# Optimization experiments

Measured on AMD Instinct MI355X. Metric: run time of the kernel, lower is better.

The kernel has to match this reference:

```python
import jax, jax.numpy as jnp
import numpy as np

S = 16        # neighbor samples per layer
NL = 2        # number of GNN layers


def setup_inputs() -> dict:
    key = jax.random.key(0)
    ks = jax.random.split(key, 12)
    N_NODES, D, E, NMP, DEG, N_EDGE, B, NC = 50000, 128, 32, 3, 32, 200000, 1024, 8
    sc = 0.05
    return {
        "ids": jax.random.randint(ks[0], (B,), 0, N_NODES, dtype=jnp.int32),
        "feats": jax.random.normal(ks[1], (N_NODES, D), jnp.float32),
        "edge_emb": jax.random.normal(ks[2], (NMP, N_EDGE, E), jnp.float32),
        "adj_nodes": jax.random.randint(ks[3], (NMP, N_NODES, DEG), 0, N_NODES, dtype=jnp.int32),
        "adj_edges": jax.random.randint(ks[4], (NMP, N_NODES, DEG), 0, N_EDGE, dtype=jnp.int32),
        "W_self": jax.random.normal(ks[5], (NMP, NL, D, D), jnp.float32) * sc,
        "W_neigh": jax.random.normal(ks[6], (NMP, NL, D + E, D), jnp.float32) * sc,
        "W_edge": jax.random.normal(ks[7], (NMP, NL, 2 * D + E, E), jnp.float32) * sc,
        "attn": jax.random.normal(ks[8], (D,), jnp.float32) * sc,
        "fc_w": jax.random.normal(ks[9], (D, NC), jnp.float32) * sc,
        "fc_b": jnp.zeros((NC,), jnp.float32),
    }


def reference(ids, feats, edge_emb, adj_nodes, adj_edges, W_self, W_neigh, W_edge, attn, fc_w, fc_b):
    NMP = adj_nodes.shape[0]
    outs = []
    for mp in range(NMP):
        # --- sample neighbor tree (deterministic: first S columns) ---
        cur = ids
        all_feats = [feats[cur]]
        all_edges = []
        for _ in range(NL):
            nb = adj_nodes[mp][cur][:, :S].reshape(-1)     # [N*S]
            eid = adj_edges[mp][cur][:, :S].reshape(-1)    # [N*S]
            all_edges.append(edge_emb[mp][eid])            # [N*S, E]
            cur = nb
            all_feats.append(feats[cur])
        # --- per-layer aggregation + edge update ---
        for l in range(NL):
            new_feats = []
            for k in range(len(all_feats) - 1):
                xs, xn, ee = all_feats[k], all_feats[k + 1], all_edges[k]
                N = xs.shape[0]
                # mean over sampled neighbors of [neigh_feat || edge_emb]
                nin = jnp.concatenate(
                    [xn.reshape(N, S, -1), ee.reshape(N, S, -1)], axis=-1
                ).mean(axis=1)                             # [N, D+E]
                new_feats.append(jax.nn.relu(xs @ W_self[mp, l] + nin @ W_neigh[mp, l]))
            all_feats = new_feats  # dropout is identity in eval mode
            new_edges = []
            for k in range(len(all_edges) - 1):
                xs, xn, ee = all_feats[k], all_feats[k + 1], all_edges[k]
                rep = jnp.repeat(xs, S, axis=0)            # [N*S, D]
                new_edges.append(jax.nn.relu(
                    jnp.concatenate([rep, xn, ee], axis=-1) @ W_edge[mp, l]))
            all_edges = new_edges
        outs.append(all_feats[0])                          # [B, D]
    stacked = jnp.stack(outs)                              # [NMP, B, D]
    # metapath attention fuse
    scores = jnp.tanh(jnp.einsum('mbd,d->mb', stacked, attn))
    beta = jax.nn.softmax(scores, axis=0)
    emb = jnp.einsum('mb,mbd->bd', beta, stacked)          # [B, D]
    # F.normalize(dim=1)
    emb = emb / jnp.maximum(jnp.linalg.norm(emb, axis=1, keepdims=True), 1e-12)
    return emb @ fc_w + fc_b
```

## Files before the change

### kernel.cpp

```cpp
#include <hip/hip_runtime.h>

#define NNODES  50000
#define D       128
#define E       32
#define NMP     3
#define DEG     32
#define NEDGE   200000
#define B       1024
#define NC      8
#define S       16

#define RPM      17408
#define NKT      9
#define WSTRIDE  36864
#define WESTRIDE 9216

typedef float f4 __attribute__((ext_vector_type(4)));
typedef short bh8 __attribute__((ext_vector_type(8)));

static __device__ __forceinline__ unsigned short f2bf(float f) {
    unsigned int u = __float_as_uint(f);
    u = u + 0x7FFFu + ((u >> 16) & 1u);
    return (unsigned short)(u >> 16);
}
static __device__ __forceinline__ float bf2f(unsigned short h) {
    return __uint_as_float(((unsigned int)h) << 16);
}

__global__ __launch_bounds__(256) void convert_k(
    const float* __restrict__ feats, const float* __restrict__ Ws,
    const float* __restrict__ Wn, const float* __restrict__ We,
    unsigned short* __restrict__ fb, unsigned short* __restrict__ WT0,
    unsigned short* __restrict__ WTe)
{
    int i = blockIdx.x * 256 + threadIdx.x;
    if (i < 1600000) {
        float4 v = ((const float4*)feats)[i];
        unsigned int p0 = (unsigned int)f2bf(v.x) | ((unsigned int)f2bf(v.y) << 16);
        unsigned int p1 = (unsigned int)f2bf(v.z) | ((unsigned int)f2bf(v.w) << 16);
        ((uint2*)fb)[i] = make_uint2(p0, p1);
    } else if (i < 1600000 + 6 * WSTRIDE) {
        int i2 = i - 1600000;
        int ml = i2 / WSTRIDE, e = i2 % WSTRIDE;
        int j = e & 7, t1 = e >> 3;
        int n = t1 & 127, t2 = t1 >> 7;
        int q = t2 & 3, kt = t2 >> 2;
        int k = kt * 32 + q * 8 + j;
        float v = (k < 128) ? Ws[((size_t)ml * 128 + k) * 128 + n]
                            : Wn[((size_t)ml * 160 + (k - 128)) * 128 + n];
        WT0[(size_t)ml * WSTRIDE + e] = f2bf(v);
    } else if (i < 1600000 + 6 * WSTRIDE + 3 * WESTRIDE) {
        int i3 = i - 1600000 - 6 * WSTRIDE;
        int mp = i3 / WESTRIDE, e = i3 % WESTRIDE;
        int j = e & 7, t1 = e >> 3;
        int n = t1 & 31, t2 = t1 >> 5;
        int q = t2 & 3, kt = t2 >> 2;
        int k = kt * 32 + q * 8 + j;
        float v = We[(((size_t)mp * 2) * 288 + k) * 32 + n];
        WTe[(size_t)mp * WESTRIDE + e] = f2bf(v);
    }
}

__global__ __launch_bounds__(256) void sample_k(
    const int* __restrict__ ids, const int* __restrict__ adjn,
    const int* __restrict__ adje, int* __restrict__ gx, int* __restrict__ eid1)
{
    int mp = blockIdx.y;
    int i = blockIdx.x * 256 + threadIdx.x;
    const int* an = adjn + (size_t)mp * NNODES * DEG;
    const int* ae = adje + (size_t)mp * NNODES * DEG;
    if (i < 16384) {
        int node = ids[i >> 4];
        gx[mp * RPM + i]     = an[(size_t)node * DEG + (i & 15)];
        eid1[mp * 16384 + i] = ae[(size_t)node * DEG + (i & 15)];
    } else if (i < RPM) {
        gx[mp * RPM + i] = ids[i - 16384];
    }
}

__global__ __launch_bounds__(256) void aggnin_k(
    const unsigned short* __restrict__ fb, const float* __restrict__ edge_emb,
    const int* __restrict__ adjn, const int* __restrict__ adje,
    const int* __restrict__ gx, const int* __restrict__ eid1,
    unsigned short* __restrict__ nin)
{
    const int mp = blockIdx.y;
    const int r = blockIdx.x * 4 + (threadIdx.x >> 6);
    const int t = threadIdx.x & 63;
    const float* ee = edge_emb + (size_t)mp * NEDGE * E;

    const int* ip;
    const int* eix;
    if (r < 16384) {
        int node = __builtin_amdgcn_readfirstlane(gx[mp * RPM + r]);
        ip  = adjn + ((size_t)mp * NNODES + node) * DEG;
        eix = adje + ((size_t)mp * NNODES + node) * DEG;
    } else {
        ip  = gx + mp * RPM + (r - 16384) * S;
        eix = eid1 + mp * 16384 + (r - 16384) * S;
    }

    const int hi = t >> 5, t31 = t & 31;

    unsigned int fv[S];
#pragma unroll
    for (int j = 0; j < S; ++j) {
        int nb = __builtin_amdgcn_readfirstlane(ip[j]);
        fv[j] = ((const unsigned int*)fb)[(size_t)nb * 64 + t];
    }
    float ev[S / 2];
#pragma unroll
    for (int e = 0; e < S / 2; ++e) {
        int e_ev = __builtin_amdgcn_readfirstlane(eix[2 * e]);
        int e_od = __builtin_amdgcn_readfirstlane(eix[2 * e + 1]);
        int edd = hi ? e_od : e_ev;
        ev[e] = ee[(size_t)edd * E + t31];
    }

    float s0 = 0.f, s1 = 0.f, se = 0.f;
#pragma unroll
    for (int j = 0; j < S; ++j) {
        s0 += bf2f((unsigned short)(fv[j] & 0xFFFF));
        s1 += bf2f((unsigned short)(fv[j] >> 16));
    }
#pragma unroll
    for (int e = 0; e < S / 2; ++e) se += ev[e];
    se += __shfl_xor(se, 32);

    const float inv = 1.0f / (float)S;
    unsigned short* row = nin + ((size_t)mp * RPM + r) * 160;
    ((unsigned int*)row)[t] =
        (unsigned int)f2bf(s0 * inv) | ((unsigned int)f2bf(s1 * inv) << 16);
    if (t < E) row[128 + t] = f2bf(se * inv);
}

__global__ __launch_bounds__(256) void gemm_feat_k(
    const unsigned short* __restrict__ fb, const int* __restrict__ gx,
    const unsigned short* __restrict__ fout_in,
    const unsigned short* __restrict__ nin,
    const unsigned short* __restrict__ WT0,
    unsigned short* __restrict__ outb, float* __restrict__ outf, int mode)
{
    const int mp = blockIdx.y;
    const int w = threadIdx.x >> 6;
    const int l = threadIdx.x & 63;
    const int q = l >> 4, lm = l & 15;
    const int m0 = blockIdx.x * 128 + w * 32;
    const int ninStride = mode ? B : RPM;
    const unsigned short* wb = WT0 + ((size_t)mp * 2 + mode) * WSTRIDE;

    const unsigned short* ap[2];
    const unsigned short* np[2];
#pragma unroll
    for (int mt = 0; mt < 2; ++mt) {
        int row = m0 + mt * 16 + lm;
        if (mode == 0) {
            int node = gx[mp * RPM + row];
            ap[mt] = fb + (size_t)node * 128;
        } else {
            ap[mt] = fout_in + ((size_t)mp * RPM + 16384 + row) * 128;
        }
        np[mt] = nin + ((size_t)mp * ninStride + row) * 160;
    }

    f4 acc[2][8];
#pragma unroll
    for (int mt = 0; mt < 2; ++mt)
#pragma unroll
        for (int nt = 0; nt < 8; ++nt) acc[mt][nt] = (f4){0.f, 0.f, 0.f, 0.f};

#pragma unroll
    for (int kt = 0; kt < NKT; ++kt) {
        const int k0 = kt * 32 + q * 8;
        bh8 a[2];
#pragma unroll
        for (int mt = 0; mt < 2; ++mt) {
            const unsigned short* p = (k0 < 128) ? (ap[mt] + k0) : (np[mt] + (k0 - 128));
            a[mt] = *(const bh8*)p;
        }
        const unsigned short* wrow = wb + ((size_t)(kt * 4 + q) * 128 + lm) * 8;
#pragma unroll
        for (int nt = 0; nt < 8; ++nt) {
            bh8 bf = *(const bh8*)(wrow + nt * 16 * 8);
#pragma unroll
            for (int mt = 0; mt < 2; ++mt)
                acc[mt][nt] = __builtin_amdgcn_mfma_f32_16x16x32_bf16(a[mt], bf, acc[mt][nt], 0, 0, 0);
        }
    }

    if (mode == 0) {
#pragma unroll
        for (int mt = 0; mt < 2; ++mt)
#pragma unroll
            for (int nt = 0; nt < 8; ++nt)
#pragma unroll
                for (int rr = 0; rr < 4; ++rr) {
                    int row = m0 + mt * 16 + q * 4 + rr;
                    int col = nt * 16 + lm;
                    outb[((size_t)mp * RPM + row) * 128 + col] = f2bf(fmaxf(acc[mt][nt][rr], 0.f));
                }
    } else {
#pragma unroll
        for (int mt = 0; mt < 2; ++mt)
#pragma unroll
            for (int nt = 0; nt < 8; ++nt)
#pragma unroll
                for (int rr = 0; rr < 4; ++rr) {
                    int row = m0 + mt * 16 + q * 4 + rr;
                    int col = nt * 16 + lm;
                    outf[((size_t)mp * B + row) * 128 + col] = fmaxf(acc[mt][nt][rr], 0.f);
                }
    }
}

__global__ __launch_bounds__(256) void gemm_edge_k(
    const unsigned short* __restrict__ fout, const float* __restrict__ edge_emb,
    const int* __restrict__ eid1, const unsigned short* __restrict__ WTe,
    unsigned short* __restrict__ e0p)
{
    const int mp = blockIdx.y;
    const int w = threadIdx.x >> 6, l = threadIdx.x & 63;
    const int q = l >> 4, lm = l & 15;
    const int m0 = blockIdx.x * 128 + w * 32;
    const unsigned short* we = WTe + (size_t)mp * WESTRIDE;
    const unsigned short* f1base = fout + (size_t)mp * RPM * 128;
    const unsigned short* f0base = fout + ((size_t)mp * RPM + 16384) * 128;
    const float* ee = edge_emb + (size_t)mp * NEDGE * E;

    const unsigned short* a1p[2];
    const unsigned short* a0p[2];
    int eidL[2];
#pragma unroll
    for (int mt = 0; mt < 2; ++mt) {
        int row = m0 + mt * 16 + lm;
        a1p[mt] = f1base + (size_t)row * 128;
        a0p[mt] = f0base + (size_t)(row >> 4) * 128;
        eidL[mt] = eid1[mp * 16384 + row];
    }

    f4 acc[2][2];
#pragma unroll
    for (int mt = 0; mt < 2; ++mt) { acc[mt][0] = (f4){0,0,0,0}; acc[mt][1] = (f4){0,0,0,0}; }

#pragma unroll
    for (int kt = 0; kt < NKT; ++kt) {
        const int k0 = kt * 32 + q * 8;
        bh8 a[2];
#pragma unroll
        for (int mt = 0; mt < 2; ++mt) {
            if (kt < 4) {
                a[mt] = *(const bh8*)(a0p[mt] + k0);
            } else if (kt < 8) {
                a[mt] = *(const bh8*)(a1p[mt] + (k0 - 128));
            } else {
                const float* ep = ee + (size_t)eidL[mt] * E + q * 8;
                float4 v0 = *(const float4*)ep;
                float4 v1 = *(const float4*)(ep + 4);
                bh8 tv;
                tv[0] = (short)f2bf(v0.x); tv[1] = (short)f2bf(v0.y);
                tv[2] = (short)f2bf(v0.z); tv[3] = (short)f2bf(v0.w);
                tv[4] = (short)f2bf(v1.x); tv[5] = (short)f2bf(v1.y);
                tv[6] = (short)f2bf(v1.z); tv[7] = (short)f2bf(v1.w);
                a[mt] = tv;
            }
        }
        const unsigned short* wrow = we + ((size_t)(kt * 4 + q) * 32 + lm) * 8;
        bh8 b0 = *(const bh8*)(wrow);
        bh8 b1 = *(const bh8*)(wrow + 16 * 8);
#pragma unroll
        for (int mt = 0; mt < 2; ++mt) {
            acc[mt][0] = __builtin_amdgcn_mfma_f32_16x16x32_bf16(a[mt], b0, acc[mt][0], 0, 0, 0);
            acc[mt][1] = __builtin_amdgcn_mfma_f32_16x16x32_bf16(a[mt], b1, acc[mt][1], 0, 0, 0);
        }
    }
#pragma unroll
    for (int mt = 0; mt < 2; ++mt)
#pragma unroll
        for (int nt = 0; nt < 2; ++nt)
#pragma unroll
            for (int rr = 0; rr < 4; ++rr) {
                int row = m0 + mt * 16 + q * 4 + rr;
                int col = nt * 16 + lm;
                e0p[((size_t)mp * 16384 + row) * 32 + col] = f2bf(fmaxf(acc[mt][nt][rr], 0.f));
            }
}

__global__ __launch_bounds__(256) void aggseq_k(
    const unsigned short* __restrict__ fout, const unsigned short* __restrict__ e0p,
    unsigned short* __restrict__ agg1)
{
    int mp = blockIdx.y;
    int bRow = blockIdx.x * 4 + (threadIdx.x >> 6);
    int t = threadIdx.x & 63;
    const unsigned short* f1 = fout + ((size_t)mp * RPM + (size_t)bRow * 16) * 128;
    const unsigned short* e0 = e0p + ((size_t)mp * 16384 + (size_t)bRow * 16) * 32;
    float s0 = 0.f, s1 = 0.f, se = 0.f;
#pragma unroll
    for (int j = 0; j < S; ++j) {
        unsigned int u = ((const unsigned int*)(f1 + j * 128))[t];
        s0 += bf2f((unsigned short)(u & 0xFFFF));
        s1 += bf2f((unsigned short)(u >> 16));
        if (t < E) se += bf2f(e0[j * 32 + t]);
    }
    const float inv = 1.0f / (float)S;
    unsigned short* row = agg1 + ((size_t)mp * B + bRow) * 160;
    ((unsigned int*)row)[t] =
        (unsigned int)f2bf(s0 * inv) | ((unsigned int)f2bf(s1 * inv) << 16);
    if (t < E) row[128 + t] = f2bf(se * inv);
}

__global__ __launch_bounds__(64) void finalize_k(
    const float* __restrict__ outs,
    const float* __restrict__ attn, const float* __restrict__ fcw,
    const float* __restrict__ fcb, float* __restrict__ out)
{
    const int b = blockIdx.x;
    const int t = threadIdx.x;
    float v0[NMP], v1[NMP], sc[NMP];
    float at0 = attn[t], at1 = attn[64 + t];
#pragma unroll
    for (int mp = 0; mp < NMP; ++mp) {
        v0[mp] = outs[((size_t)mp * B + b) * D + t];
        v1[mp] = outs[((size_t)mp * B + b) * D + 64 + t];
        float p = v0[mp] * at0 + v1[mp] * at1;
#pragma unroll
        for (int off = 32; off; off >>= 1) p += __shfl_xor(p, off);
        sc[mp] = tanhf(p);
    }
    float mx = fmaxf(sc[0], fmaxf(sc[1], sc[2]));
    float e0 = expf(sc[0] - mx), e1 = expf(sc[1] - mx), e2 = expf(sc[2] - mx);
    float isum = 1.f / (e0 + e1 + e2);
    float b0 = e0 * isum, b1 = e1 * isum, b2 = e2 * isum;
    float emb0 = b0 * v0[0] + b1 * v0[1] + b2 * v0[2];
    float emb1 = b0 * v1[0] + b1 * v1[1] + b2 * v1[2];
    float nn = emb0 * emb0 + emb1 * emb1;
#pragma unroll
    for (int off = 32; off; off >>= 1) nn += __shfl_xor(nn, off);
    float innorm = 1.f / fmaxf(sqrtf(nn), 1e-12f);
    emb0 *= innorm; emb1 *= innorm;
    float pc[NC];
#pragma unroll
    for (int c = 0; c < NC; ++c) {
        float p = emb0 * fcw[t * NC + c] + emb1 * fcw[(64 + t) * NC + c];
#pragma unroll
        for (int off = 32; off; off >>= 1) p += __shfl_xor(p, off);
        pc[c] = p;
    }
    if (t == 0) {
#pragma unroll
        for (int c = 0; c < NC; ++c)
            out[(size_t)b * NC + c] = pc[c] + fcb[c];
    }
}

extern "C" void kernel_launch(void* const* d_in, const int* in_sizes, int n_in,
                              void* d_out, int out_size, void* d_ws, size_t ws_size,
                              hipStream_t stream) {
    const int* ids        = (const int*)d_in[0];
    const float* feats    = (const float*)d_in[1];
    const float* edge_emb = (const float*)d_in[2];
    const int* adjn       = (const int*)d_in[3];
    const int* adje       = (const int*)d_in[4];
    const float* Ws       = (const float*)d_in[5];
    const float* Wn       = (const float*)d_in[6];
    const float* We       = (const float*)d_in[7];
    const float* attn     = (const float*)d_in[8];
    const float* fcw      = (const float*)d_in[9];
    const float* fcb      = (const float*)d_in[10];
    float* out = (float*)d_out;

    char* p = (char*)d_ws;
    unsigned short* WT0 = (unsigned short*)p; p += (size_t)6 * WSTRIDE * 2;
    unsigned short* WTe = (unsigned short*)p; p += (size_t)3 * WESTRIDE * 2;
    unsigned short* fb  = (unsigned short*)p; p += (size_t)NNODES * 128 * 2;
    int* gx   = (int*)p;                      p += (size_t)3 * RPM * 4;
    int* eid1 = (int*)p;                      p += (size_t)3 * 16384 * 4;
    unsigned short* nin  = (unsigned short*)p; p += (size_t)3 * RPM * 160 * 2;
    unsigned short* fout = (unsigned short*)p; p += (size_t)3 * RPM * 128 * 2;
    unsigned short* e0p  = (unsigned short*)p; p += (size_t)3 * 16384 * 32 * 2;
    unsigned short* agg1 = (unsigned short*)p; p += (size_t)3 * B * 160 * 2;
    float* outs = (float*)p;                   p += (size_t)3 * B * 128 * 4;

    convert_k<<<7222, 256, 0, stream>>>(feats, Ws, Wn, We, fb, WT0, WTe);
    sample_k<<<dim3(68, 3), 256, 0, stream>>>(ids, adjn, adje, gx, eid1);
    aggnin_k<<<dim3(RPM / 4, 3), 256, 0, stream>>>(fb, edge_emb, adjn, adje, gx, eid1, nin);
    gemm_feat_k<<<dim3(136, 3), 256, 0, stream>>>(fb, gx, fout, nin, WT0, fout, nullptr, 0);
    gemm_edge_k<<<dim3(128, 3), 256, 0, stream>>>(fout, edge_emb, eid1, WTe, e0p);
    aggseq_k<<<dim3(256, 3), 256, 0, stream>>>(fout, e0p, agg1);
    gemm_feat_k<<<dim3(8, 3), 256, 0, stream>>>(fb, nullptr, fout, agg1, WT0, nullptr, outs, 1);
    finalize_k<<<B, 64, 0, stream>>>(outs, attn, fcw, fcb, out);
}
```

Baseline: 248.2 us.

## Fuse pipeline stages to cut kernel launches and intermediate buffers

Merges weight/feature conversion with neighbor sampling into one launch. Folds the edge-GEMM output straight into the mean aggregation, so the e0p intermediate buffer is never written. Combines the final layer's feature GEMM with the attention, normalize and FC finalize step through shared memory, dropping the outs buffer. This goes from eight launches to five and removes intermediate global traffic, but the final fused kernel runs only 32 blocks, which limits parallelism on that stage.

```diff
diff --git a/kernel.cpp b/kernel.cpp
--- a/kernel.cpp
+++ b/kernel.cpp
@@ -15,6 +15,9 @@
 #define WSTRIDE  36864
 #define WESTRIDE 9216
 
+#define CONV_TASKS (1600000 + 6 * WSTRIDE + 3 * WESTRIDE)
+#define TOT_TASKS  (CONV_TASKS + 3 * RPM)
+
 typedef float f4 __attribute__((ext_vector_type(4)));
 typedef short bh8 __attribute__((ext_vector_type(8)));
 
@@ -27,11 +30,13 @@
     return __uint_as_float(((unsigned int)h) << 16);
 }
 
-__global__ __launch_bounds__(256) void convert_k(
+__global__ __launch_bounds__(256) void convsamp_k(
     const float* __restrict__ feats, const float* __restrict__ Ws,
     const float* __restrict__ Wn, const float* __restrict__ We,
+    const int* __restrict__ ids, const int* __restrict__ adjn,
+    const int* __restrict__ adje,
     unsigned short* __restrict__ fb, unsigned short* __restrict__ WT0,
-    unsigned short* __restrict__ WTe)
+    unsigned short* __restrict__ WTe, int* __restrict__ gx, int* __restrict__ eid1)
 {
     int i = blockIdx.x * 256 + threadIdx.x;
     if (i < 1600000) {
@@ -49,7 +54,7 @@
         float v = (k < 128) ? Ws[((size_t)ml * 128 + k) * 128 + n]
                             : Wn[((size_t)ml * 160 + (k - 128)) * 128 + n];
         WT0[(size_t)ml * WSTRIDE + e] = f2bf(v);
-    } else if (i < 1600000 + 6 * WSTRIDE + 3 * WESTRIDE) {
+    } else if (i < CONV_TASKS) {
         int i3 = i - 1600000 - 6 * WSTRIDE;
         int mp = i3 / WESTRIDE, e = i3 % WESTRIDE;
         int j = e & 7, t1 = e >> 3;
@@ -58,23 +63,16 @@
         int k = kt * 32 + q * 8 + j;
         float v = We[(((size_t)mp * 2) * 288 + k) * 32 + n];
         WTe[(size_t)mp * WESTRIDE + e] = f2bf(v);
-    }
-}
-
-__global__ __launch_bounds__(256) void sample_k(
-    const int* __restrict__ ids, const int* __restrict__ adjn,
-    const int* __restrict__ adje, int* __restrict__ gx, int* __restrict__ eid1)
-{
-    int mp = blockIdx.y;
-    int i = blockIdx.x * 256 + threadIdx.x;
-    const int* an = adjn + (size_t)mp * NNODES * DEG;
-    const int* ae = adje + (size_t)mp * NNODES * DEG;
-    if (i < 16384) {
-        int node = ids[i >> 4];
-        gx[mp * RPM + i]     = an[(size_t)node * DEG + (i & 15)];
-        eid1[mp * 16384 + i] = ae[(size_t)node * DEG + (i & 15)];
-    } else if (i < RPM) {
-        gx[mp * RPM + i] = ids[i - 16384];
+    } else if (i < TOT_TASKS) {
+        int i4 = i - CONV_TASKS;
+        int mp = i4 / RPM, r = i4 % RPM;
+        if (r < 16384) {
+            int node = ids[r >> 4];
+            gx[mp * RPM + r]   = adjn[((size_t)mp * NNODES + node) * DEG + (r & 15)];
+            eid1[mp * 16384 + r] = adje[((size_t)mp * NNODES + node) * DEG + (r & 15)];
+        } else {
+            gx[mp * RPM + r] = ids[r - 16384];
+        }
     }
 }
 
@@ -136,31 +134,25 @@
 
 __global__ __launch_bounds__(256) void gemm_feat_k(
     const unsigned short* __restrict__ fb, const int* __restrict__ gx,
-    const unsigned short* __restrict__ fout_in,
     const unsigned short* __restrict__ nin,
     const unsigned short* __restrict__ WT0,
-    unsigned short* __restrict__ outb, float* __restrict__ outf, int mode)
+    unsigned short* __restrict__ outb)
 {
     const int mp = blockIdx.y;
     const int w = threadIdx.x >> 6;
     const int l = threadIdx.x & 63;
     const int q = l >> 4, lm = l & 15;
     const int m0 = blockIdx.x * 128 + w * 32;
-    const int ninStride = mode ? B : RPM;
-    const unsigned short* wb = WT0 + ((size_t)mp * 2 + mode) * WSTRIDE;
+    const unsigned short* wb = WT0 + (size_t)mp * 2 * WSTRIDE;
 
     const unsigned short* ap[2];
     const unsigned short* np[2];
 #pragma unroll
     for (int mt = 0; mt < 2; ++mt) {
         int row = m0 + mt * 16 + lm;
-        if (mode == 0) {
-            int node = gx[mp * RPM + row];
-            ap[mt] = fb + (size_t)node * 128;
-        } else {
-            ap[mt] = fout_in + ((size_t)mp * RPM + 16384 + row) * 128;
-        }
-        np[mt] = nin + ((size_t)mp * ninStride + row) * 160;
+        int node = gx[mp * RPM + row];
+        ap[mt] = fb + (size_t)node * 128;
+        np[mt] = nin + ((size_t)mp * RPM + row) * 160;
     }
 
     f4 acc[2][8];
@@ -188,35 +180,22 @@
         }
     }
 
-    if (mode == 0) {
-#pragma unroll
-        for (int mt = 0; mt < 2; ++mt)
-#pragma unroll
-            for (int nt = 0; nt < 8; ++nt)
-#pragma unroll
-                for (int rr = 0; rr < 4; ++rr) {
-                    int row = m0 + mt * 16 + q * 4 + rr;
-                    int col = nt * 16 + lm;
-                    outb[((size_t)mp * RPM + row) * 128 + col] = f2bf(fmaxf(acc[mt][nt][rr], 0.f));
-                }
-    } else {
-#pragma unroll
-        for (int mt = 0; mt < 2; ++mt)
-#pragma unroll
-            for (int nt = 0; nt < 8; ++nt)
-#pragma unroll
-                for (int rr = 0; rr < 4; ++rr) {
-                    int row = m0 + mt * 16 + q * 4 + rr;
-                    int col = nt * 16 + lm;
-                    outf[((size_t)mp * B + row) * 128 + col] = fmaxf(acc[mt][nt][rr], 0.f);
-                }
-    }
-}
-
-__global__ __launch_bounds__(256) void gemm_edge_k(
+#pragma unroll
+    for (int mt = 0; mt < 2; ++mt)
+#pragma unroll
+        for (int nt = 0; nt < 8; ++nt)
+#pragma unroll
+            for (int rr = 0; rr < 4; ++rr) {
+                int row = m0 + mt * 16 + q * 4 + rr;
+                int col = nt * 16 + lm;
+                outb[((size_t)mp * RPM + row) * 128 + col] = f2bf(fmaxf(acc[mt][nt][rr], 0.f));
+            }
+}
+
+__global__ __launch_bounds__(256) void edgeagg_k(
     const unsigned short* __restrict__ fout, const float* __restrict__ edge_emb,
     const int* __restrict__ eid1, const unsigned short* __restrict__ WTe,
-    unsigned short* __restrict__ e0p)
+    unsigned short* __restrict__ agg1)
 {
     const int mp = blockIdx.y;
     const int w = threadIdx.x >> 6, l = threadIdx.x & 63;
@@ -226,6 +205,7 @@
     const unsigned short* f1base = fout + (size_t)mp * RPM * 128;
     const unsigned short* f0base = fout + ((size_t)mp * RPM + 16384) * 128;
     const float* ee = edge_emb + (size_t)mp * NEDGE * E;
+    const float inv = 1.0f / (float)S;
 
     const unsigned short* a1p[2];
     const unsigned short* a0p[2];
@@ -273,83 +253,116 @@
             acc[mt][1] = __builtin_amdgcn_mfma_f32_16x16x32_bf16(a[mt], b1, acc[mt][1], 0, 0, 0);
         }
     }
-#pragma unroll
-    for (int mt = 0; mt < 2; ++mt)
-#pragma unroll
-        for (int nt = 0; nt < 2; ++nt)
-#pragma unroll
-            for (int rr = 0; rr < 4; ++rr) {
-                int row = m0 + mt * 16 + q * 4 + rr;
-                int col = nt * 16 + lm;
-                e0p[((size_t)mp * 16384 + row) * 32 + col] = f2bf(fmaxf(acc[mt][nt][rr], 0.f));
-            }
-}
-
-__global__ __launch_bounds__(256) void aggseq_k(
-    const unsigned short* __restrict__ fout, const unsigned short* __restrict__ e0p,
-    unsigned short* __restrict__ agg1)
-{
-    int mp = blockIdx.y;
-    int bRow = blockIdx.x * 4 + (threadIdx.x >> 6);
-    int t = threadIdx.x & 63;
-    const unsigned short* f1 = fout + ((size_t)mp * RPM + (size_t)bRow * 16) * 128;
-    const unsigned short* e0 = e0p + ((size_t)mp * 16384 + (size_t)bRow * 16) * 32;
-    float s0 = 0.f, s1 = 0.f, se = 0.f;
-#pragma unroll
-    for (int j = 0; j < S; ++j) {
-        unsigned int u = ((const unsigned int*)(f1 + j * 128))[t];
-        s0 += bf2f((unsigned short)(u & 0xFFFF));
-        s1 += bf2f((unsigned short)(u >> 16));
-        if (t < E) se += bf2f(e0[j * 32 + t]);
-    }
-    const float inv = 1.0f / (float)S;
-    unsigned short* row = agg1 + ((size_t)mp * B + bRow) * 160;
-    ((unsigned int*)row)[t] =
-        (unsigned int)f2bf(s0 * inv) | ((unsigned int)f2bf(s1 * inv) << 16);
-    if (t < E) row[128 + t] = f2bf(se * inv);
-}
-
-__global__ __launch_bounds__(64) void finalize_k(
-    const float* __restrict__ outs,
+
+#pragma unroll
+    for (int mt = 0; mt < 2; ++mt) {
+        int seg = (m0 >> 4) + mt;
+#pragma unroll
+        for (int nt = 0; nt < 2; ++nt) {
+            float ps = 0.f;
+#pragma unroll
+            for (int rr = 0; rr < 4; ++rr) ps += fmaxf(acc[mt][nt][rr], 0.f);
+            ps += __shfl_xor(ps, 16);
+            ps += __shfl_xor(ps, 32);
+            if (l < 16)
+                agg1[((size_t)mp * B + seg) * 160 + 128 + nt * 16 + lm] = f2bf(ps * inv);
+        }
+    }
+
+#pragma unroll
+    for (int mt = 0; mt < 2; ++mt) {
+        int seg = (m0 >> 4) + mt;
+        const unsigned short* fr = f1base + (size_t)seg * 16 * 128;
+        float s0 = 0.f, s1 = 0.f;
+#pragma unroll
+        for (int j = 0; j < S; ++j) {
+            unsigned int u = ((const unsigned int*)(fr + j * 128))[l];
+            s0 += bf2f((unsigned short)(u & 0xFFFF));
+            s1 += bf2f((unsigned short)(u >> 16));
+        }
+        ((unsigned int*)(agg1 + ((size_t)mp * B + seg) * 160))[l] =
+            (unsigned int)f2bf(s0 * inv) | ((unsigned int)f2bf(s1 * inv) << 16);
+    }
+}
+
+__global__ __launch_bounds__(256) void feat1fin_k(
+    const unsigned short* __restrict__ fout, const unsigned short* __restrict__ agg1,
+    const unsigned short* __restrict__ WT0,
     const float* __restrict__ attn, const float* __restrict__ fcw,
     const float* __restrict__ fcb, float* __restrict__ out)
 {
-    const int b = blockIdx.x;
-    const int t = threadIdx.x;
-    float v0[NMP], v1[NMP], sc[NMP];
-    float at0 = attn[t], at1 = attn[64 + t];
+    __shared__ float sbuf[NMP][32][132];
+    const int w = threadIdx.x >> 6, l = threadIdx.x & 63;
+    const int q = l >> 4, lm = l & 15;
+    const int m0 = blockIdx.x * 32;
+
+    for (int task = w; task < 6; task += 4) {
+        const int mp = task >> 1, mt = task & 1;
+        const int row = m0 + mt * 16 + lm;
+        const unsigned short* ap = fout + ((size_t)mp * RPM + 16384 + row) * 128;
+        const unsigned short* np = agg1 + ((size_t)mp * B + row) * 160;
+        const unsigned short* wb = WT0 + ((size_t)mp * 2 + 1) * WSTRIDE;
+
+        f4 acc[8];
+#pragma unroll
+        for (int nt = 0; nt < 8; ++nt) acc[nt] = (f4){0.f, 0.f, 0.f, 0.f};
+#pragma unroll
+        for (int kt = 0; kt < NKT; ++kt) {
+            const int k0 = kt * 32 + q * 8;
+            bh8 a = (k0 < 128) ? *(const bh8*)(ap + k0) : *(const bh8*)(np + (k0 - 128));
+            const unsigned short* wrow = wb + ((size_t)(kt * 4 + q) * 128 + lm) * 8;
+#pragma unroll
+            for (int nt = 0; nt < 8; ++nt) {
+                bh8 bf = *(const bh8*)(wrow + nt * 16 * 8);
+                acc[nt] = __builtin_amdgcn_mfma_f32_16x16x32_bf16(a, bf, acc[nt], 0, 0, 0);
+            }
+        }
+#pragma unroll
+        for (int nt = 0; nt < 8; ++nt)
+#pragma unroll
+            for (int rr = 0; rr < 4; ++rr)
+                sbuf[mp][mt * 16 + q * 4 + rr][nt * 16 + lm] = fmaxf(acc[nt][rr], 0.f);
+    }
+    __syncthreads();
+
+    const int row = threadIdx.x >> 3;
+    const int j = threadIdx.x & 7;
+    const int d0 = j * 16;
+    float sc[NMP];
 #pragma unroll
     for (int mp = 0; mp < NMP; ++mp) {
-        v0[mp] = outs[((size_t)mp * B + b) * D + t];
-        v1[mp] = outs[((size_t)mp * B + b) * D + 64 + t];
-        float p = v0[mp] * at0 + v1[mp] * at1;
-#pragma unroll
-        for (int off = 32; off; off >>= 1) p += __shfl_xor(p, off);
+        float p = 0.f;
+#pragma unroll
+        for (int d = 0; d < 16; ++d) p += sbuf[mp][row][d0 + d] * attn[d0 + d];
+        p += __shfl_xor(p, 1); p += __shfl_xor(p, 2); p += __shfl_xor(p, 4);
         sc[mp] = tanhf(p);
     }
     float mx = fmaxf(sc[0], fmaxf(sc[1], sc[2]));
     float e0 = expf(sc[0] - mx), e1 = expf(sc[1] - mx), e2 = expf(sc[2] - mx);
     float isum = 1.f / (e0 + e1 + e2);
     float b0 = e0 * isum, b1 = e1 * isum, b2 = e2 * isum;
-    float emb0 = b0 * v0[0] + b1 * v0[1] + b2 * v0[2];
-    float emb1 = b0 * v1[0] + b1 * v1[1] + b2 * v1[2];
-    float nn = emb0 * emb0 + emb1 * emb1;
-#pragma unroll
-    for (int off = 32; off; off >>= 1) nn += __shfl_xor(nn, off);
+
+    float emb[16];
+    float nn = 0.f;
+#pragma unroll
+    for (int d = 0; d < 16; ++d) {
+        float v = b0 * sbuf[0][row][d0 + d] + b1 * sbuf[1][row][d0 + d]
+                + b2 * sbuf[2][row][d0 + d];
+        emb[d] = v;
+        nn += v * v;
+    }
+    nn += __shfl_xor(nn, 1); nn += __shfl_xor(nn, 2); nn += __shfl_xor(nn, 4);
     float innorm = 1.f / fmaxf(sqrtf(nn), 1e-12f);
-    emb0 *= innorm; emb1 *= innorm;
-    float pc[NC];
+#pragma unroll
+    for (int d = 0; d < 16; ++d) emb[d] *= innorm;
+
 #pragma unroll
     for (int c = 0; c < NC; ++c) {
-        float p = emb0 * fcw[t * NC + c] + emb1 * fcw[(64 + t) * NC + c];
-#pragma unroll
-        for (int off = 32; off; off >>= 1) p += __shfl_xor(p, off);
-        pc[c] = p;
-    }
-    if (t == 0) {
-#pragma unroll
-        for (int c = 0; c < NC; ++c)
-            out[(size_t)b * NC + c] = pc[c] + fcb[c];
+        float p = 0.f;
+#pragma unroll
+        for (int d = 0; d < 16; ++d) p += emb[d] * fcw[(d0 + d) * NC + c];
+        p += __shfl_xor(p, 1); p += __shfl_xor(p, 2); p += __shfl_xor(p, 4);
+        if (j == c) out[(size_t)(m0 + row) * NC + c] = p + fcb[c];
     }
 }
 
@@ -377,16 +390,12 @@
     int* eid1 = (int*)p;                      p += (size_t)3 * 16384 * 4;
     unsigned short* nin  = (unsigned short*)p; p += (size_t)3 * RPM * 160 * 2;
     unsigned short* fout = (unsigned short*)p; p += (size_t)3 * RPM * 128 * 2;
-    unsigned short* e0p  = (unsigned short*)p; p += (size_t)3 * 16384 * 32 * 2;
     unsigned short* agg1 = (unsigned short*)p; p += (size_t)3 * B * 160 * 2;
-    float* outs = (float*)p;                   p += (size_t)3 * B * 128 * 4;
-
-    convert_k<<<7222, 256, 0, stream>>>(feats, Ws, Wn, We, fb, WT0, WTe);
-    sample_k<<<dim3(68, 3), 256, 0, stream>>>(ids, adjn, adje, gx, eid1);
+
+    convsamp_k<<<TOT_TASKS / 256, 256, 0, stream>>>(feats, Ws, Wn, We, ids, adjn, adje,
+                                                    fb, WT0, WTe, gx, eid1);
     aggnin_k<<<dim3(RPM / 4, 3), 256, 0, stream>>>(fb, edge_emb, adjn, adje, gx, eid1, nin);
-    gemm_feat_k<<<dim3(136, 3), 256, 0, stream>>>(fb, gx, fout, nin, WT0, fout, nullptr, 0);
-    gemm_edge_k<<<dim3(128, 3), 256, 0, stream>>>(fout, edge_emb, eid1, WTe, e0p);
-    aggseq_k<<<dim3(256, 3), 256, 0, stream>>>(fout, e0p, agg1);
-    gemm_feat_k<<<dim3(8, 3), 256, 0, stream>>>(fb, nullptr, fout, agg1, WT0, nullptr, outs, 1);
-    finalize_k<<<B, 64, 0, stream>>>(outs, attn, fcw, fcb, out);
-}
+    gemm_feat_k<<<dim3(136, 3), 256, 0, stream>>>(fb, gx, nin, WT0, fout);
+    edgeagg_k<<<dim3(128, 3), 256, 0, stream>>>(fout, edge_emb, eid1, WTe, agg1);
+    feat1fin_k<<<32, 256, 0, stream>>>(fout, agg1, WT0, attn, fcw, fcb, out);
+}
```

Measured after the change: 253.1 us. About the same (+2.0%).
